# Performance work log

Hardware: AMD Instinct MI355X
Metric: run time of the kernel (lower is better)

Reference implementation:

```python
import jax, jax.numpy as jnp
import numpy as np

V, E, H, L, C = 50257, 256, 256, 2, 64
B, T = 4, 48
MASK_ID = 103
EPS = 1e-5
SAMPLE_KEY = jax.random.key(1234)


def lstm_cell(x, h, c, Wih, Whh, bih, bhh):
    # PyTorch gate order: i, f, g, o
    z = x @ Wih.T + h @ Whh.T + (bih + bhh)  # [B,4H]
    i, f, g, o = jnp.split(z, 4, axis=-1)
    c = jax.nn.sigmoid(f) * c + jax.nn.sigmoid(i) * jnp.tanh(g)
    h = jax.nn.sigmoid(o) * jnp.tanh(c)
    return h, c


def setup_inputs() -> dict:
    key = jax.random.key(0)
    ks = jax.random.split(key, 16)
    g = lambda k, s: (jax.random.normal(k, s, dtype=jnp.float32) * 0.05)
    emb = g(ks[0], (V, E)).at[0].set(0.0)  # padding_idx=0 row zeroed
    params = dict(
        emb=emb,
        W_e2e=g(ks[1], (H, E)), b_e2e=jnp.zeros((H,), jnp.float32),
        W_e2d=g(ks[2], (H, E)), b_e2d=jnp.zeros((H,), jnp.float32),
        enc_Wih=g(ks[3], (L, 4 * H, H)), enc_Whh=g(ks[4], (L, 4 * H, H)),
        enc_bih=jnp.zeros((L, 4 * H), jnp.float32), enc_bhh=jnp.zeros((L, 4 * H), jnp.float32),
        dec_Wih=g(ks[5], (L, 4 * H, H)), dec_Whh=g(ks[6], (L, 4 * H, H)),
        dec_bih=jnp.zeros((L, 4 * H), jnp.float32), dec_bhh=jnp.zeros((L, 4 * H), jnp.float32),
        W_cls=g(ks[7], (C, 1)), b_cls=jnp.zeros((C,), jnp.float32),
        W_fc1=g(ks[8], (H + C, H + C)), b_fc1=jnp.zeros((H + C,), jnp.float32),
        ln_g=jnp.ones((H + C,), jnp.float32), ln_b=jnp.zeros((H + C,), jnp.float32),
        W_fc2=g(ks[9], (V, H + C)), b_fc2=jnp.zeros((V,), jnp.float32),
    )
    input_ids = jax.random.randint(ks[10], (B, T), 0, V, dtype=jnp.int32)
    mask_pos = jax.random.bernoulli(ks[11], 0.3, (B, T))  # ensure masked slots exist
    input_ids = jnp.where(mask_pos, jnp.int32(MASK_ID), input_ids)
    attention_mask = jnp.ones((B, T), jnp.int32)
    classification_labels = jax.random.bernoulli(ks[12], 0.5, (B,)).astype(jnp.float32)
    return dict(input_ids=input_ids, attention_mask=attention_mask,
                classification_labels=classification_labels, **params)


def _forward(input_ids, classification_labels, emb, W_e2e, b_e2e, W_e2d, b_e2d,
             enc_Wih, enc_Whh, enc_bih, enc_bhh, dec_Wih, dec_Whh, dec_bih, dec_bhh,
             W_cls, b_cls, W_fc1, b_fc1, ln_g, ln_b, W_fc2, b_fc2):
    f32 = jnp.float32
    # ---- encoder: embed -> linear+relu (dropout=eval identity) -> 2-layer LSTM ----
    xe = jax.nn.relu(emb[input_ids] @ W_e2e.T + b_e2e)  # [B,T,H]
    xs = jnp.swapaxes(xe, 0, 1)  # [T,B,H]
    h0 = jnp.zeros((L, B, H), f32)

    def enc_step(hc, xj):
        h, c = hc
        cur, hs, cs = xj, [], []
        for l in range(L):
            nh, nc = lstm_cell(cur, h[l], c[l], enc_Wih[l], enc_Whh[l], enc_bih[l], enc_bhh[l])
            hs.append(nh); cs.append(nc); cur = nh
        return (jnp.stack(hs), jnp.stack(cs)), None

    (h, c), _ = jax.lax.scan(enc_step, (h0, h0), xs)

    # classifier states are loop-invariant in the original (hoisted, same math)
    cls_states = classification_labels[:, None] @ W_cls.T + b_cls  # [B,C]

    tokens0 = jnp.zeros((B, T), input_ids.dtype).at[:, 0].set(input_ids[:, 0])

    def decode_step(carry, t):
        tokens, h, c = carry
        # re-embed the ENTIRE current prefix, as the original does each step
        x = jax.nn.relu(emb[tokens] @ W_e2d.T + b_e2d)  # [B,T,H]
        xs_t = jnp.swapaxes(x, 0, 1)  # [T,B,H]

        def mstep(hc, inp):
            hh, cc = hc
            xj, j = inp
            cur, hs, cs = xj, [], []
            for l in range(L):
                nh, nc = lstm_cell(cur, hh[l], cc[l], dec_Wih[l], dec_Whh[l], dec_bih[l], dec_bhh[l])
                hs.append(nh); cs.append(nc); cur = nh
            nh, nc = jnp.stack(hs), jnp.stack(cs)
            valid = j < t  # only positions 0..t-1 are real prefix tokens
            hh = jnp.where(valid, nh, hh)
            cc = jnp.where(valid, nc, cc)
            return (hh, cc), hh[-1]

        (h, c), ys = jax.lax.scan(mstep, (h, c), (xs_t, jnp.arange(T)))
        dec_out = jax.lax.dynamic_index_in_dim(ys, t - 1, axis=0, keepdims=False)  # [B,H]

        z = jnp.concatenate([dec_out, cls_states], axis=-1)  # [B,H+C]
        z1 = jax.nn.relu(z @ W_fc1.T + b_fc1)
        mu = z1.mean(-1, keepdims=True)
        var = ((z1 - mu) ** 2).mean(-1, keepdims=True)
        z1 = (z1 - mu) * jax.lax.rsqrt(var + EPS) * ln_g + ln_b
        logits = z1 @ W_fc2.T + b_fc2  # [B,V]
        logp = jax.nn.log_softmax(logits, axis=-1)

        gumb = jax.random.gumbel(jax.random.fold_in(SAMPLE_KEY, t), logp.shape)
        sampled = jnp.argmax(logp + gumb, axis=-1)  # [B] categorical sample
        slp = jnp.take_along_axis(logp, sampled[:, None], axis=-1)[:, 0]  # [B]

        cur_tok = jnp.take(input_ids, t, axis=1)  # [B]
        next_tok = jnp.where(cur_tok == MASK_ID, sampled.astype(tokens.dtype), cur_tok)
        tokens = jax.lax.dynamic_update_slice(tokens, next_tok[:, None], (0, t))
        return (tokens, h, c), slp

    (tokens, h, c), slps = jax.lax.scan(decode_step, (tokens0, h, c), jnp.arange(1, T))
    scores = jnp.concatenate([jnp.zeros((B, 1), f32), slps.T], axis=1)  # [B,T]
    return scores, tokens


def reference(input_ids, attention_mask, classification_labels, emb, W_e2e, b_e2e,
              W_e2d, b_e2d, enc_Wih, enc_Whh, enc_bih, enc_bhh, dec_Wih, dec_Whh,
              dec_bih, dec_bhh, W_cls, b_cls, W_fc1, b_fc1, ln_g, ln_b, W_fc2, b_fc2):
    # attention_mask is accepted but unused, matching the original forward
    return _forward(input_ids, classification_labels, emb, W_e2e, b_e2e, W_e2d, b_e2d,
                    enc_Wih, enc_Whh, enc_bih, enc_bhh, dec_Wih, dec_Whh, dec_bih, dec_bhh,
                    W_cls, b_cls, W_fc1, b_fc1, ln_g, ln_b, W_fc2, b_fc2)
```

## Files before the change

kernel.cpp:

```cpp
#include <hip/hip_runtime.h>
#include <stdint.h>
#include <stddef.h>
#include <math.h>


#define PARTITIONABLE_PRNG 1

namespace s2sr {

constexpr int kV = 50257, kE = 256, kH = 256, kCc = 64, kB = 4, kT = 48;
constexpr int kZ = kH + kCc;
constexpr int kG = 4 * kH;
constexpr int kMask = 103;
constexpr float kEps = 1e-5f;
constexpr float kTiny = 1.17549435e-38f;

constexpr int NWG = 256, TPB = 256;
constexpr int NCL = 32;
constexpr int LEAD = 32;
constexpr int GANG0 = 33;
constexpr int NGANG = NWG - GANG0;
constexpr int RPW = (kV + NGANG - 1) / NGANG;
constexpr int NPX = 16;

constexpr int SH_H0 = 0;
constexpr int SH_H1 = 1024;
constexpr int SH_P0 = 2048;
constexpr int SH_P1 = 3072;
constexpr int SH_TOT = 4608;
constexpr int LD_ZIN = 0;
constexpr int LD_Z1  = 1280;
constexpr int LD_CLS = 2560;
constexpr int LD_LSE = 2816;
constexpr int LD_WPS = 2820;

struct alignas(128) Tag { unsigned v; unsigned _p[31]; };
struct alignas(128) GOut {
  unsigned long long key[kB];
  float ps[kB];
  unsigned tag;
  unsigned _p[19];
};

struct SyncBlk {
  Tag ictr, igen;
  Tag ptok4[NPX][4];
  Tag ztag4[4];
  Tag etok4[4];
  Tag hztag[NCL];
  GOut gout[NGANG];
};

struct WS {
  SyncBlk s;
  unsigned long long hc0[2][kB * kH];
  unsigned long long hc1[2][kB * kH];
  float hzbuf[2][kB][kH];
  float z1n[2][kB][kZ];
  float xcur[kB][kH];
  float xd0[kB][kH];
  float px0[kT][kB][kG];
  float pxe[kT][kB][kG];
};

__device__ __forceinline__ float aldf(const float* p) {
  return __hip_atomic_load(p, __ATOMIC_RELAXED, __HIP_MEMORY_SCOPE_AGENT);
}
__device__ __forceinline__ void astf(float* p, float v) {
  __hip_atomic_store(p, v, __ATOMIC_RELAXED, __HIP_MEMORY_SCOPE_AGENT);
}
__device__ __forceinline__ unsigned ldu(const unsigned* p) {
  return __hip_atomic_load(p, __ATOMIC_RELAXED, __HIP_MEMORY_SCOPE_AGENT);
}
__device__ __forceinline__ unsigned long long ld64(const unsigned long long* p) {
  return __hip_atomic_load(p, __ATOMIC_RELAXED, __HIP_MEMORY_SCOPE_AGENT);
}
__device__ __forceinline__ void st64(unsigned long long* p, unsigned long long v) {
  __hip_atomic_store(p, v, __ATOMIC_RELAXED, __HIP_MEMORY_SCOPE_AGENT);
}
__device__ __forceinline__ void relTag(Tag* tg, unsigned v) {
  __hip_atomic_store(&tg->v, v, __ATOMIC_RELEASE, __HIP_MEMORY_SCOPE_AGENT);
}
__device__ __forceinline__ void gbar(SyncBlk* sb, unsigned tgt) {
  __syncthreads();
  if (threadIdx.x == 0) {
    const unsigned old = __hip_atomic_fetch_add(&sb->ictr.v, 1u, __ATOMIC_RELEASE,
                                                __HIP_MEMORY_SCOPE_AGENT);
    if (old == tgt - 1u) relTag(&sb->igen, tgt);
    while (ldu(&sb->igen.v) < tgt) __builtin_amdgcn_s_sleep(2);
    __atomic_signal_fence(__ATOMIC_ACQUIRE);
  }
  __syncthreads();
}

__device__ __forceinline__ unsigned rotl32(unsigned v, int n) {
  return (v << n) | (v >> (32 - n));
}
__device__ __forceinline__ void tf2x32(unsigned k0, unsigned k1, unsigned x0, unsigned x1,
                                       unsigned& o0, unsigned& o1) {
  const unsigned k2 = k0 ^ k1 ^ 0x1BD11BDAu;
  unsigned v0 = x0 + k0, v1 = x1 + k1;
  v0 += v1; v1 = rotl32(v1, 13); v1 ^= v0;
  v0 += v1; v1 = rotl32(v1, 15); v1 ^= v0;
  v0 += v1; v1 = rotl32(v1, 26); v1 ^= v0;
  v0 += v1; v1 = rotl32(v1, 6);  v1 ^= v0;
  v0 += k1; v1 += k2 + 1u;
  v0 += v1; v1 = rotl32(v1, 17); v1 ^= v0;
  v0 += v1; v1 = rotl32(v1, 29); v1 ^= v0;
  v0 += v1; v1 = rotl32(v1, 16); v1 ^= v0;
  v0 += v1; v1 = rotl32(v1, 24); v1 ^= v0;
  v0 += k2; v1 += k0 + 2u;
  v0 += v1; v1 = rotl32(v1, 13); v1 ^= v0;
  v0 += v1; v1 = rotl32(v1, 15); v1 ^= v0;
  v0 += v1; v1 = rotl32(v1, 26); v1 ^= v0;
  v0 += v1; v1 = rotl32(v1, 6);  v1 ^= v0;
  v0 += k0; v1 += k1 + 3u;
  v0 += v1; v1 = rotl32(v1, 17); v1 ^= v0;
  v0 += v1; v1 = rotl32(v1, 29); v1 ^= v0;
  v0 += v1; v1 = rotl32(v1, 16); v1 ^= v0;
  v0 += v1; v1 = rotl32(v1, 24); v1 ^= v0;
  v0 += k1; v1 += k2 + 4u;
  v0 += v1; v1 = rotl32(v1, 13); v1 ^= v0;
  v0 += v1; v1 = rotl32(v1, 15); v1 ^= v0;
  v0 += v1; v1 = rotl32(v1, 26); v1 ^= v0;
  v0 += v1; v1 = rotl32(v1, 6);  v1 ^= v0;
  o0 = v0 + k2; o1 = v1 + k0 + 5u;
}
__device__ __forceinline__ unsigned rbits(unsigned k0, unsigned k1, unsigned i) {
#if PARTITIONABLE_PRNG
  unsigned a, b; tf2x32(k0, k1, 0u, i, a, b);
  return a ^ b;
#else
  constexpr unsigned HALF = (unsigned)((kB * kV + 1) / 2);
  unsigned a, b;
  if (i < HALF) { tf2x32(k0, k1, i, i + HALF, a, b); return a; }
  tf2x32(k0, k1, i - HALF, i, a, b); return b;
#endif
}
__device__ __forceinline__ float gumbel_from_bits(unsigned bits) {
  float f = __uint_as_float((bits >> 9) | 0x3f800000u) - 1.0f;
  f = fmaxf(f, kTiny);
  return -logf(-logf(f));
}
__device__ __forceinline__ unsigned ordkey(float f) {
  const unsigned u = __float_as_uint(f);
  return (u & 0x80000000u) ? ~u : (u | 0x80000000u);
}
__device__ __forceinline__ unsigned long long shflx64(unsigned long long v, int m) {
  unsigned lo = (unsigned)v, hi = (unsigned)(v >> 32);
  lo = (unsigned)__shfl_xor((int)lo, m, 64);
  hi = (unsigned)__shfl_xor((int)hi, m, 64);
  return ((unsigned long long)hi << 32) | (unsigned long long)lo;
}
__device__ __forceinline__ float sigm(float x) { return 1.0f / (1.0f + expf(-x)); }

template <bool STREAM>
__device__ __forceinline__ void lstm_tick(
    WS* ws, float* shf, int cw, int cc, bool do0, bool do1,
    const float* px, const float* pW0, const float* pW1,
    const float4* w0r, const float4* w1r,
    const float* bs0, const float* bs1,
    float& c0, float& c1, float& h0last, float& h1last,
    int w, int r, bool fin, int fu, int fb, int hzt) {
  const int tid = (int)threadIdx.x;
  float pxg0 = 0.f, pxg1 = 0.f, pxg2 = 0.f, pxg3 = 0.f;
  if (do0 && fin) {
    const float* pb = px + fb * kG + cw * 8 + fu;
    pxg0 = aldf(pb);
    pxg1 = aldf(pb + 256);
    pxg2 = aldf(pb + 512);
    pxg3 = aldf(pb + 768);
  }
  {
    const unsigned long long* base = &ws->hc0[(cc + 1) & 1][0];
    const unsigned expseq = (unsigned)cc;
    unsigned long long v[4];
#pragma unroll
    for (int k = 0; k < 4; ++k) v[k] = ld64(base + tid + k * 256);
    unsigned pend = 0;
#pragma unroll
    for (int k = 0; k < 4; ++k) if ((unsigned)v[k] != expseq) pend |= 1u << k;
    while (pend) {
#pragma unroll
      for (int k = 0; k < 4; ++k)
        if (pend & (1u << k)) v[k] = ld64(base + tid + k * 256);
#pragma unroll
      for (int k = 0; k < 4; ++k)
        if ((unsigned)v[k] == expseq) pend &= ~(1u << k);
    }
#pragma unroll
    for (int k = 0; k < 4; ++k)
      shf[SH_H0 + tid + k * 256] = __uint_as_float((unsigned)(v[k] >> 32));
  }
  __syncthreads();
  if (do0) {
    float4 wv0[8];
#pragma unroll
    for (int i = 0; i < 8; ++i)
      wv0[i] = STREAM ? *reinterpret_cast<const float4*>(pW0 + i * 4) : w0r[i];
    const float* A = &shf[SH_H0 + w * 32];
    float a0 = 0.f, a1 = 0.f, a2 = 0.f, a3 = 0.f;
#pragma unroll
    for (int i = 0; i < 8; ++i) {
      const float4 wv = wv0[i];
      const float4 x0 = *reinterpret_cast<const float4*>(A + 0 * 256 + i * 4);
      const float4 x1 = *reinterpret_cast<const float4*>(A + 1 * 256 + i * 4);
      const float4 x2 = *reinterpret_cast<const float4*>(A + 2 * 256 + i * 4);
      const float4 x3 = *reinterpret_cast<const float4*>(A + 3 * 256 + i * 4);
      a0 = fmaf(wv.x, x0.x, a0); a0 = fmaf(wv.y, x0.y, a0); a0 = fmaf(wv.z, x0.z, a0); a0 = fmaf(wv.w, x0.w, a0);
      a1 = fmaf(wv.x, x1.x, a1); a1 = fmaf(wv.y, x1.y, a1); a1 = fmaf(wv.z, x1.z, a1); a1 = fmaf(wv.w, x1.w, a1);
      a2 = fmaf(wv.x, x2.x, a2); a2 = fmaf(wv.y, x2.y, a2); a2 = fmaf(wv.z, x2.z, a2); a2 = fmaf(wv.w, x2.w, a2);
      a3 = fmaf(wv.x, x3.x, a3); a3 = fmaf(wv.y, x3.y, a3); a3 = fmaf(wv.z, x3.z, a3); a3 = fmaf(wv.w, x3.w, a3);
    }
    *reinterpret_cast<float4*>(&shf[SH_P0 + w * 128 + r * 4]) = float4{a0, a1, a2, a3};
  }
  __syncthreads();
  if (fin) {
    float hn = h0last;
    if (do0) {
      float z[4];
#pragma unroll
      for (int g = 0; g < 4; ++g) {
        const int base2 = SH_P0 + (fu * 4 + g) * 4 + fb;
        z[g] = shf[base2 + 0 * 128] + shf[base2 + 1 * 128] + shf[base2 + 2 * 128] +
               shf[base2 + 3 * 128] + shf[base2 + 4 * 128] + shf[base2 + 5 * 128] +
               shf[base2 + 6 * 128] + shf[base2 + 7 * 128] + bs0[g];
      }
      z[0] += pxg0; z[1] += pxg1; z[2] += pxg2; z[3] += pxg3;
      const float cn = sigm(z[1]) * c0 + sigm(z[0]) * tanhf(z[2]);
      hn = sigm(z[3]) * tanhf(cn);
      c0 = cn;
    }
    h0last = hn;
    st64(&ws->hc0[cc & 1][fb * 256 + cw * 8 + fu],
         ((unsigned long long)__float_as_uint(hn) << 32) |
         (unsigned long long)(unsigned)(cc + 1));
  }
  {
    const unsigned long long* base = &ws->hc1[(cc + 1) & 1][0];
    const unsigned expseq = (unsigned)cc;
    unsigned long long v[4];
#pragma unroll
    for (int k = 0; k < 4; ++k) v[k] = ld64(base + tid + k * 256);
    unsigned pend = 0;
#pragma unroll
    for (int k = 0; k < 4; ++k) if ((unsigned)v[k] != expseq) pend |= 1u << k;
    while (pend) {
#pragma unroll
      for (int k = 0; k < 4; ++k)
        if (pend & (1u << k)) v[k] = ld64(base + tid + k * 256);
#pragma unroll
      for (int k = 0; k < 4; ++k)
        if ((unsigned)v[k] == expseq) pend &= ~(1u << k);
    }
#pragma unroll
    for (int k = 0; k < 4; ++k)
      shf[SH_H1 + tid + k * 256] = __uint_as_float((unsigned)(v[k] >> 32));
  }
  __syncthreads();
  if (do1) {
    float4 wv1[16];
#pragma unroll
    for (int i = 0; i < 16; ++i)
      wv1[i] = STREAM ? *reinterpret_cast<const float4*>(pW1 + i * 4) : w1r[i];
    const float* Bp = (w < 4) ? &shf[SH_H0 + w * 64] : &shf[SH_H1 + (w - 4) * 64];
    float a0 = 0.f, a1 = 0.f, a2 = 0.f, a3 = 0.f;
#pragma unroll
    for (int i = 0; i < 16; ++i) {
      const float4 wv = wv1[i];
      const float4 x0 = *reinterpret_cast<const float4*>(Bp + 0 * 256 + i * 4);
      const float4 x1 = *reinterpret_cast<const float4*>(Bp + 1 * 256 + i * 4);
      const float4 x2 = *reinterpret_cast<const float4*>(Bp + 2 * 256 + i * 4);
      const float4 x3 = *reinterpret_cast<const float4*>(Bp + 3 * 256 + i * 4);
      a0 = fmaf(wv.x, x0.x, a0); a0 = fmaf(wv.y, x0.y, a0); a0 = fmaf(wv.z, x0.z, a0); a0 = fmaf(wv.w, x0.w, a0);
      a1 = fmaf(wv.x, x1.x, a1); a1 = fmaf(wv.y, x1.y, a1); a1 = fmaf(wv.z, x1.z, a1); a1 = fmaf(wv.w, x1.w, a1);
      a2 = fmaf(wv.x, x2.x, a2); a2 = fmaf(wv.y, x2.y, a2); a2 = fmaf(wv.z, x2.z, a2); a2 = fmaf(wv.w, x2.w, a2);
      a3 = fmaf(wv.x, x3.x, a3); a3 = fmaf(wv.y, x3.y, a3); a3 = fmaf(wv.z, x3.z, a3); a3 = fmaf(wv.w, x3.w, a3);
    }
    *reinterpret_cast<float4*>(&shf[SH_P1 + w * 128 + r * 4]) = float4{a0, a1, a2, a3};
  }
  __syncthreads();
  if (fin) {
    float hn = h1last;
    if (do1) {
      float z[4];
#pragma unroll
      for (int g = 0; g < 4; ++g) {
        const int base2 = SH_P1 + (fu * 4 + g) * 4 + fb;
        z[g] = shf[base2 + 0 * 128] + shf[base2 + 1 * 128] + shf[base2 + 2 * 128] +
               shf[base2 + 3 * 128] + shf[base2 + 4 * 128] + shf[base2 + 5 * 128] +
               shf[base2 + 6 * 128] + shf[base2 + 7 * 128] + bs1[g];
      }
      const float cn = sigm(z[1]) * c1 + sigm(z[0]) * tanhf(z[2]);
      hn = sigm(z[3]) * tanhf(cn);
      c1 = cn;
    }
    h1last = hn;
    st64(&ws->hc1[cc & 1][fb * 256 + cw * 8 + fu],
         ((unsigned long long)__float_as_uint(hn) << 32) |
         (unsigned long long)(unsigned)(cc + 1));
    if (hzt >= 0) astf(&ws->hzbuf[hzt & 1][fb][cw * 8 + fu], hn);
  }
}

__global__ void __launch_bounds__(TPB, 1) s2s_kernel(
    const int* __restrict__ input_ids, const float* __restrict__ labels,
    const float* __restrict__ emb,
    const float* __restrict__ W_e2e, const float* __restrict__ b_e2e,
    const float* __restrict__ W_e2d, const float* __restrict__ b_e2d,
    const float* __restrict__ encWih, const float* __restrict__ encWhh,
    const float* __restrict__ encbih, const float* __restrict__ encbhh,
    const float* __restrict__ decWih, const float* __restrict__ decWhh,
    const float* __restrict__ decbih, const float* __restrict__ decbhh,
    const float* __restrict__ W_cls, const float* __restrict__ b_cls,
    const float* __restrict__ Wfc1, const float* __restrict__ bfc1,
    const float* __restrict__ lng, const float* __restrict__ lnb,
    const float* __restrict__ W_fc2, const float* __restrict__ b_fc2,
    float* __restrict__ out, WS* __restrict__ ws) {
  const int wg = (int)blockIdx.x;
  const int tid = (int)threadIdx.x;
  SyncBlk* sb = &ws->s;
  __shared__ __align__(16) float shf[SH_TOT];
  __shared__ unsigned long long shk[16];
  __shared__ int shi[8];

  if (wg < kB * kT) {
    const int b = wg / kT, j = wg % kT;
    const int id = input_ids[b * kT + j];
    for (int i = tid; i < kE; i += 256) shf[i] = emb[(size_t)id * kE + i];
    __syncthreads();
    const float* wr = W_e2e + (size_t)tid * kE;
    float acc = b_e2e[tid];
    for (int k = 0; k < kE; k += 4) {
      const float4 wv = *reinterpret_cast<const float4*>(wr + k);
      const float4 xv = *reinterpret_cast<const float4*>(&shf[k]);
      acc = fmaf(xv.x, wv.x, acc); acc = fmaf(xv.y, wv.y, acc);
      acc = fmaf(xv.z, wv.z, acc); acc = fmaf(xv.w, wv.w, acc);
    }
    __syncthreads();
    shf[256 + tid] = fmaxf(acc, 0.f);
  } else if (wg == 192) {
    if (tid < kB) {
      const int t0 = input_ids[tid * kT];
      out[tid * kT] = 0.f;
      out[kB * kT + tid * kT] = (float)t0;
    }
  } else if (wg == 193) {
    const float* wr = W_e2d + (size_t)tid * kE;
    const float* e0 = emb + (size_t)input_ids[0 * kT] * kE;
    const float* e1 = emb + (size_t)input_ids[1 * kT] * kE;
    const float* e2 = emb + (size_t)input_ids[2 * kT] * kE;
    const float* e3 = emb + (size_t)input_ids[3 * kT] * kE;
    const float bb = b_e2d[tid];
    float a0 = bb, a1 = bb, a2 = bb, a3 = bb;
    for (int k = 0; k < kE; k += 4) {
      const float4 wv = *reinterpret_cast<const float4*>(wr + k);
      const float4 v0 = *reinterpret_cast<const float4*>(e0 + k);
      const float4 v1 = *reinterpret_cast<const float4*>(e1 + k);
      const float4 v2 = *reinterpret_cast<const float4*>(e2 + k);
      const float4 v3 = *reinterpret_cast<const float4*>(e3 + k);
      a0 = fmaf(v0.x, wv.x, a0); a0 = fmaf(v0.y, wv.y, a0); a0 = fmaf(v0.z, wv.z, a0); a0 = fmaf(v0.w, wv.w, a0);
      a1 = fmaf(v1.x, wv.x, a1); a1 = fmaf(v1.y, wv.y, a1); a1 = fmaf(v1.z, wv.z, a1); a1 = fmaf(v1.w, wv.w, a1);
      a2 = fmaf(v2.x, wv.x, a2); a2 = fmaf(v2.y, wv.y, a2); a2 = fmaf(v2.z, wv.z, a2); a2 = fmaf(v2.w, wv.w, a2);
      a3 = fmaf(v3.x, wv.x, a3); a3 = fmaf(v3.y, wv.y, a3); a3 = fmaf(v3.z, wv.z, a3); a3 = fmaf(v3.w, wv.w, a3);
    }
    astf(&ws->xd0[0][tid], fmaxf(a0, 0.f));
    astf(&ws->xd0[1][tid], fmaxf(a1, 0.f));
    astf(&ws->xd0[2][tid], fmaxf(a2, 0.f));
    astf(&ws->xd0[3][tid], fmaxf(a3, 0.f));
  }
  gbar(sb, (unsigned)NWG);

  if (wg < kB * kT) {
    const int b = wg / kT, j = wg % kT;
#pragma unroll
    for (int rr = 0; rr < 4; ++rr) {
      const int g = rr * 256 + tid;
      const float* wr = encWih + (size_t)g * kH;
      float acc = 0.f;
      for (int k = 0; k < kH; k += 4) {
        const float4 wv = *reinterpret_cast<const float4*>(wr + k);
        const float4 xv = *reinterpret_cast<const float4*>(&shf[256 + k]);
        acc = fmaf(xv.x, wv.x, acc); acc = fmaf(xv.y, wv.y, acc);
        acc = fmaf(xv.z, wv.z, acc); acc = fmaf(xv.w, wv.w, acc);
      }
      astf(&ws->pxe[j][0][0] + (size_t)b * kG + g, acc);
    }
  } else if (wg >= 192 && wg < 208) {
    const int w2 = wg - 192, b = w2 >> 2, q = w2 & 3;
    const int g = q * 256 + tid;
    for (int i = tid; i < kH; i += 256) shf[i] = aldf(&ws->xd0[b][i]);
    __syncthreads();
    const float* wr = decWih + (size_t)g * kH;
    float acc = 0.f;
    for (int k = 0; k < kH; k += 4) {
      const float4 wv = *reinterpret_cast<const float4*>(wr + k);
      const float4 xv = *reinterpret_cast<const float4*>(&shf[k]);
      acc = fmaf(xv.x, wv.x, acc); acc = fmaf(xv.y, wv.y, acc);
      acc = fmaf(xv.z, wv.z, acc); acc = fmaf(xv.w, wv.w, acc);
    }
    astf(&ws->px0[0][0][0] + (size_t)b * kG + g, acc);
  }
  gbar(sb, (unsigned)(2 * NWG));

  if (wg < NCL) {
    const int cw = wg;
    const int r = tid & 31, w = tid >> 5;
    const int grow = (r & 3) * 256 + cw * 8 + (r >> 2);
    const bool fin = tid < 32;
    const int fu = tid >> 2, fb = tid & 3;
    float c0 = 0.f, c1 = 0.f, h0last = 0.f, h1last = 0.f;
    float bs0[4] = {0.f, 0.f, 0.f, 0.f}, bs1[4] = {0.f, 0.f, 0.f, 0.f};
    if (fin) {
#pragma unroll
      for (int g = 0; g < 4; ++g) {
        bs0[g] = encbih[g * 256 + cw * 8 + fu] + encbhh[g * 256 + cw * 8 + fu];
        bs1[g] = encbih[kG + g * 256 + cw * 8 + fu] + encbhh[kG + g * 256 + cw * 8 + fu];
      }
    }
    const float* pW0e = encWhh + (size_t)grow * kH + w * 32;
    const float* pW1e = (w < 4)
        ? encWih + (size_t)kG * kH + (size_t)grow * kH + w * 64
        : encWhh + (size_t)kG * kH + (size_t)grow * kH + (w - 4) * 64;
    int cc = 0;
    for (int j = 0; j < kT; ++j, ++cc)
      lstm_tick<true>(ws, shf, cw, cc, true, j > 0, &ws->pxe[j][0][0],
                      pW0e, pW1e, nullptr, nullptr, bs0, bs1,
                      c0, c1, h0last, h1last, w, r, fin, fu, fb, -1);
    lstm_tick<true>(ws, shf, cw, cc, false, true, nullptr,
                    pW0e, pW1e, nullptr, nullptr, bs0, bs1,
                    c0, c1, h0last, h1last, w, r, fin, fu, fb, -1);
    ++cc;
    float4 w0d[8], w1d[16];
    {
      const float* p0 = decWhh + (size_t)grow * kH + w * 32;
#pragma unroll
      for (int i = 0; i < 8; ++i) w0d[i] = *reinterpret_cast<const float4*>(p0 + i * 4);
      const float* p1 = (w < 4)
          ? decWih + (size_t)kG * kH + (size_t)grow * kH + w * 64
          : decWhh + (size_t)kG * kH + (size_t)grow * kH + (w - 4) * 64;
#pragma unroll
      for (int i = 0; i < 16; ++i) w1d[i] = *reinterpret_cast<const float4*>(p1 + i * 4);
      if (fin) {
#pragma unroll
        for (int g = 0; g < 4; ++g) {
          bs0[g] = decbih[g * 256 + cw * 8 + fu] + decbhh[g * 256 + cw * 8 + fu];
          bs1[g] = decbih[kG + g * 256 + cw * 8 + fu] + decbhh[kG + g * 256 + cw * 8 + fu];
        }
      }
    }
    for (int t = 1; t < kT; ++t) {
      for (int j = 0; j < t; ++j, ++cc) {
        const bool d1 = (j > 0) || (t >= 2);
        const int hzt = (j == 0 && t >= 2) ? (t - 1) : -1;
        if (j == t - 1 && t >= 2) {
          if (tid < 64) {
            Tag* p = &sb->ptok4[tid >> 2][tid & 3];
            while (ldu(&p->v) < (unsigned)(t - 1)) {}
            __atomic_signal_fence(__ATOMIC_ACQUIRE);
          }
          __syncthreads();
        }
        lstm_tick<false>(ws, shf, cw, cc, true, d1, &ws->px0[j][0][0],
                         nullptr, nullptr, w0d, w1d, bs0, bs1,
                         c0, c1, h0last, h1last, w, r, fin, fu, fb, hzt);
        if (hzt >= 0 && tid == 0) relTag(&sb->hztag[cw], (unsigned)hzt);
      }
    }
    lstm_tick<false>(ws, shf, cw, cc, false, true, nullptr,
                     nullptr, nullptr, w0d, w1d, bs0, bs1,
                     c0, c1, h0last, h1last, w, r, fin, fu, fb, kT - 1);
    if (tid == 0) relTag(&sb->hztag[cw], (unsigned)(kT - 1));
  } else if (wg == LEAD) {
    if (tid < kB * kCc) {
      const int b = tid >> 6, c = tid & 63;
      shf[LD_CLS + tid] = fmaf(labels[b], W_cls[c], b_cls[c]);
    }
    __syncthreads();
    for (int t = 1; t < kT; ++t) {
      if (tid < NCL) {
        while (ldu(&sb->hztag[tid].v) < (unsigned)t) __builtin_amdgcn_s_sleep(1);
        __atomic_signal_fence(__ATOMIC_ACQUIRE);
      }
      __syncthreads();
      for (int i = tid; i < kB * kZ; i += 256) {
        const int b = i / kZ, k = i - b * kZ;
        shf[LD_ZIN + i] = (k < kH) ? aldf(&ws->hzbuf[t & 1][b][k])
                                   : shf[LD_CLS + b * kCc + (k - kH)];
      }
      __syncthreads();
#pragma unroll
      for (int rep = 0; rep < 5; ++rep) {
        const int task = tid + rep * 256;
        const int b = task / kZ, o = task - b * kZ;
        const float* wr = Wfc1 + (size_t)o * kZ;
        const float* zz = &shf[LD_ZIN + b * kZ];
        float acc = bfc1[o];
        for (int k = 0; k < kZ; k += 4) {
          const float4 wv = *reinterpret_cast<const float4*>(wr + k);
          const float4 zv = *reinterpret_cast<const float4*>(zz + k);
          acc = fmaf(zv.x, wv.x, acc); acc = fmaf(zv.y, wv.y, acc);
          acc = fmaf(zv.z, wv.z, acc); acc = fmaf(zv.w, wv.w, acc);
        }
        shf[LD_Z1 + task] = fmaxf(acc, 0.f);
      }
      __syncthreads();
      {
        const int b = tid >> 6, ln = tid & 63;
        float s1 = 0.f, s2 = 0.f;
        for (int i = ln; i < kZ; i += 64) {
          const float v2 = shf[LD_Z1 + b * kZ + i]; s1 += v2; s2 += v2 * v2;
        }
#pragma unroll
        for (int o = 32; o > 0; o >>= 1) { s1 += __shfl_xor(s1, o, 64); s2 += __shfl_xor(s2, o, 64); }
        const float mu = s1 * (1.0f / kZ);
        const float var = s2 * (1.0f / kZ) - mu * mu;
        const float rs = 1.0f / sqrtf(var + kEps);
        for (int i = ln; i < kZ; i += 64) {
          const float v2 = fmaf((shf[LD_Z1 + b * kZ + i] - mu) * rs, lng[i], lnb[i]);
          shf[LD_Z1 + b * kZ + i] = v2;
          astf(&ws->z1n[t & 1][b][i], v2);
        }
        if (ln == 0) relTag(&sb->ztag4[b], (unsigned)t);
      }
      if (tid < NGANG) {
        while (ldu(&sb->gout[tid].tag) < (unsigned)t) __builtin_amdgcn_s_sleep(2);
        __atomic_signal_fence(__ATOMIC_ACQUIRE);
      }
      __syncthreads();
      {
        unsigned long long kk[kB];
        float pp[kB];
        if (tid < NGANG) {
          const GOut* g = &sb->gout[tid];
#pragma unroll
          for (int b = 0; b < kB; ++b) { kk[b] = ld64(&g->key[b]); pp[b] = aldf(&g->ps[b]); }
        } else {
#pragma unroll
          for (int b = 0; b < kB; ++b) { kk[b] = 0ull; pp[b] = 0.f; }
        }
#pragma unroll
        for (int b = 0; b < kB; ++b) {
#pragma unroll
          for (int m = 1; m < 64; m <<= 1) {
            const unsigned long long ko = shflx64(kk[b], m);
            pp[b] += __shfl_xor(pp[b], m, 64);
            if (ko > kk[b]) kk[b] = ko;
          }
        }
        if ((tid & 63) == 0) {
          const int wv = tid >> 6;
#pragma unroll
          for (int b = 0; b < kB; ++b) { shk[wv * kB + b] = kk[b]; shf[LD_WPS + wv * kB + b] = pp[b]; }
        }
      }
      __syncthreads();
      if (tid < kB) {
        const int b = tid;
        unsigned long long key = shk[b];
        float s = shf[LD_WPS + b];
        for (int wv = 1; wv < 4; ++wv) {
          const unsigned long long ko = shk[wv * kB + b];
          if (ko > key) key = ko;
          s += shf[LD_WPS + wv * kB + b];
        }
        const int samp = (int)(0xFFFFFFFFu - (unsigned)(key & 0xFFFFFFFFull));
        const float lse = logf(s);
        const int cur = input_ids[b * kT + t];
        const int nxt = (cur == kMask) ? samp : cur;
        out[kB * kT + b * kT + t] = (float)nxt;
        shi[b] = nxt; shi[4 + b] = samp;
        shf[LD_LSE + b] = lse;
      }
      __syncthreads();
      if (t < kT - 1) {
        const float* wr = W_e2d + (size_t)tid * kE;
        const float* e0 = emb + (size_t)shi[0] * kE;
        const float* e1 = emb + (size_t)shi[1] * kE;
        const float* e2 = emb + (size_t)shi[2] * kE;
        const float* e3 = emb + (size_t)shi[3] * kE;
        const float bb = b_e2d[tid];
        float a0 = bb, a1 = bb, a2 = bb, a3 = bb;
        for (int k = 0; k < kE; k += 4) {
          const float4 wv = *reinterpret_cast<const float4*>(wr + k);
          const float4 v0 = *reinterpret_cast<const float4*>(e0 + k);
          const float4 v1 = *reinterpret_cast<const float4*>(e1 + k);
          const float4 v2 = *reinterpret_cast<const float4*>(e2 + k);
          const float4 v3 = *reinterpret_cast<const float4*>(e3 + k);
          a0 = fmaf(v0.x, wv.x, a0); a0 = fmaf(v0.y, wv.y, a0); a0 = fmaf(v0.z, wv.z, a0); a0 = fmaf(v0.w, wv.w, a0);
          a1 = fmaf(v1.x, wv.x, a1); a1 = fmaf(v1.y, wv.y, a1); a1 = fmaf(v1.z, wv.z, a1); a1 = fmaf(v1.w, wv.w, a1);
          a2 = fmaf(v2.x, wv.x, a2); a2 = fmaf(v2.y, wv.y, a2); a2 = fmaf(v2.z, wv.z, a2); a2 = fmaf(v2.w, wv.w, a2);
          a3 = fmaf(v3.x, wv.x, a3); a3 = fmaf(v3.y, wv.y, a3); a3 = fmaf(v3.z, wv.z, a3); a3 = fmaf(v3.w, wv.w, a3);
        }
        astf(&ws->xcur[0][tid], fmaxf(a0, 0.f));
        astf(&ws->xcur[1][tid], fmaxf(a1, 0.f));
        astf(&ws->xcur[2][tid], fmaxf(a2, 0.f));
        astf(&ws->xcur[3][tid], fmaxf(a3, 0.f));
        if ((tid & 63) == 0) relTag(&sb->etok4[tid >> 6], (unsigned)t);
      }
      {
        const int b = tid >> 6, lane = tid & 63;
        const int sp = shi[4 + b];
        const float* wr = W_fc2 + (size_t)sp * kZ;
        float acc = 0.f;
#pragma unroll
        for (int i = 0; i < 5; ++i)
          acc = fmaf(shf[LD_Z1 + b * kZ + lane + i * 64], wr[lane + i * 64], acc);
#pragma unroll
        for (int o = 32; o > 0; o >>= 1) acc += __shfl_xor(acc, o, 64);
        if (lane == 0) out[b * kT + t] = acc + b_fc2[sp] - shf[LD_LSE + b];
      }
      __syncthreads();
    }
  } else {
    const int gi = wg - GANG0;
    const int start = gi * RPW;
    const int cnt = (RPW < kV - start) ? RPW : (kV - start);
    const bool act = tid < cnt;
    const int row = start + tid;
    for (int t = 1; t < kT; ++t) {
      if (tid < 4) {
        while (ldu(&sb->ztag4[tid].v) < (unsigned)t) __builtin_amdgcn_s_sleep(16);
        __atomic_signal_fence(__ATOMIC_ACQUIRE);
      }
      __syncthreads();
      for (int i = tid; i < kB * kZ; i += 256) shf[i] = aldf(&ws->z1n[t & 1][0][0] + i);
      __syncthreads();
      unsigned fk0, fk1;
      tf2x32(0u, 1234u, 0u, (unsigned)t, fk0, fk1);
      float lv[kB] = {0.f, 0.f, 0.f, 0.f};
      if (act) {
        const float* wr = W_fc2 + (size_t)row * kZ;
        const float bb = b_fc2[row];
// ... 119 lines not shown
```

Before: 6.969 ms.

## Split LSTM layers onto separate workgroup groups and pipeline them across ticks

```diff
diff --git a/kernel.cpp b/kernel.cpp
--- a/kernel.cpp
+++ b/kernel.cpp
@@ -16,7 +16,8 @@
 constexpr float kTiny = 1.17549435e-38f;
 
 constexpr int NWG = 256, TPB = 256;
-constexpr int NCL = 32;
+constexpr int NCL0 = 16;
+constexpr int NCL1 = 16;
 constexpr int LEAD = 32;
 constexpr int GANG0 = 33;
 constexpr int NGANG = NWG - GANG0;
@@ -25,8 +26,7 @@
 
 constexpr int SH_H0 = 0;
 constexpr int SH_H1 = 1024;
-constexpr int SH_P0 = 2048;
-constexpr int SH_P1 = 3072;
+constexpr int SH_P  = 2048;
 constexpr int SH_TOT = 4608;
 constexpr int LD_ZIN = 0;
 constexpr int LD_Z1  = 1280;
@@ -47,14 +47,14 @@
   Tag ptok4[NPX][4];
   Tag ztag4[4];
   Tag etok4[4];
-  Tag hztag[NCL];
+  Tag hztag[NCL1];
   GOut gout[NGANG];
 };
 
 struct WS {
   SyncBlk s;
-  unsigned long long hc0[2][kB * kH];
-  unsigned long long hc1[2][kB * kH];
+  unsigned long long hc0[4][kB * kH];
+  unsigned long long hc1[4][kB * kH];
   float hzbuf[2][kB][kH];
   float z1n[2][kB][kZ];
   float xcur[kB][kH];
@@ -154,65 +154,77 @@
 }
 __device__ __forceinline__ float sigm(float x) { return 1.0f / (1.0f + expf(-x)); }
 
+__device__ __forceinline__ void spin_stage(const unsigned long long* base,
+                                           unsigned expseq, float* shf, int dst) {
+  const int tid = (int)threadIdx.x;
+  unsigned long long v[4];
+#pragma unroll
+  for (int k = 0; k < 4; ++k) v[k] = ld64(base + tid + k * 256);
+  unsigned pend = 0;
+#pragma unroll
+  for (int k = 0; k < 4; ++k) if ((unsigned)v[k] != expseq) pend |= 1u << k;
+  while (pend) {
+#pragma unroll
+    for (int k = 0; k < 4; ++k)
+      if (pend & (1u << k)) v[k] = ld64(base + tid + k * 256);
+#pragma unroll
+    for (int k = 0; k < 4; ++k)
+      if ((unsigned)v[k] == expseq) pend &= ~(1u << k);
+  }
+#pragma unroll
+  for (int k = 0; k < 4; ++k)
+    shf[dst + tid + k * 256] = __uint_as_float((unsigned)(v[k] >> 32));
+}
+
 template <bool STREAM>
-__device__ __forceinline__ void lstm_tick(
-    WS* ws, float* shf, int cw, int cc, bool do0, bool do1,
-    const float* px, const float* pW0, const float* pW1,
-    const float4* w0r, const float4* w1r,
-    const float* bs0, const float* bs1,
-    float& c0, float& c1, float& h0last, float& h1last,
-    int w, int r, bool fin, int fu, int fb, int hzt) {
+__device__ __forceinline__ void l0_tick(
+    WS* ws, float* shf, int cw, int cc, bool do0, const float* px,
+    const float* pW0a, const float* pW0b, const float4* w0a, const float4* w0b,
+    const float* bs0, float& c0, float& h0last,
+    int r, int v, bool fin, int fu, int fb) {
   const int tid = (int)threadIdx.x;
   float pxg0 = 0.f, pxg1 = 0.f, pxg2 = 0.f, pxg3 = 0.f;
   if (do0 && fin) {
-    const float* pb = px + fb * kG + cw * 8 + fu;
+    const float* pb = px + fb * kG + cw * 16 + fu;
     pxg0 = aldf(pb);
     pxg1 = aldf(pb + 256);
     pxg2 = aldf(pb + 512);
     pxg3 = aldf(pb + 768);
   }
-  {
-    const unsigned long long* base = &ws->hc0[(cc + 1) & 1][0];
-    const unsigned expseq = (unsigned)cc;
-    unsigned long long v[4];
-#pragma unroll
-    for (int k = 0; k < 4; ++k) v[k] = ld64(base + tid + k * 256);
-    unsigned pend = 0;
-#pragma unroll
-    for (int k = 0; k < 4; ++k) if ((unsigned)v[k] != expseq) pend |= 1u << k;
-    while (pend) {
-#pragma unroll
-      for (int k = 0; k < 4; ++k)
-        if (pend & (1u << k)) v[k] = ld64(base + tid + k * 256);
-#pragma unroll
-      for (int k = 0; k < 4; ++k)
-        if ((unsigned)v[k] == expseq) pend &= ~(1u << k);
-    }
-#pragma unroll
-    for (int k = 0; k < 4; ++k)
-      shf[SH_H0 + tid + k * 256] = __uint_as_float((unsigned)(v[k] >> 32));
-  }
+  if (cc >= 3 && tid < NCL1) {
+    const unsigned long long* cr = &ws->hc1[(cc - 3) & 3][tid * 16];
+    const unsigned need = (unsigned)(cc - 2);
+    while ((unsigned)ld64(cr) < need) {}
+  }
+  spin_stage(&ws->hc0[(cc - 1) & 3][0], (unsigned)cc, shf, SH_H0);
   __syncthreads();
   if (do0) {
-    float4 wv0[8];
-#pragma unroll
-    for (int i = 0; i < 8; ++i)
-      wv0[i] = STREAM ? *reinterpret_cast<const float4*>(pW0 + i * 4) : w0r[i];
-    const float* A = &shf[SH_H0 + w * 32];
-    float a0 = 0.f, a1 = 0.f, a2 = 0.f, a3 = 0.f;
+    float4 wa[8], wb[8];
 #pragma unroll
     for (int i = 0; i < 8; ++i) {
-      const float4 wv = wv0[i];
-      const float4 x0 = *reinterpret_cast<const float4*>(A + 0 * 256 + i * 4);
-      const float4 x1 = *reinterpret_cast<const float4*>(A + 1 * 256 + i * 4);
-      const float4 x2 = *reinterpret_cast<const float4*>(A + 2 * 256 + i * 4);
-      const float4 x3 = *reinterpret_cast<const float4*>(A + 3 * 256 + i * 4);
-      a0 = fmaf(wv.x, x0.x, a0); a0 = fmaf(wv.y, x0.y, a0); a0 = fmaf(wv.z, x0.z, a0); a0 = fmaf(wv.w, x0.w, a0);
-      a1 = fmaf(wv.x, x1.x, a1); a1 = fmaf(wv.y, x1.y, a1); a1 = fmaf(wv.z, x1.z, a1); a1 = fmaf(wv.w, x1.w, a1);
-      a2 = fmaf(wv.x, x2.x, a2); a2 = fmaf(wv.y, x2.y, a2); a2 = fmaf(wv.z, x2.z, a2); a2 = fmaf(wv.w, x2.w, a2);
-      a3 = fmaf(wv.x, x3.x, a3); a3 = fmaf(wv.y, x3.y, a3); a3 = fmaf(wv.z, x3.z, a3); a3 = fmaf(wv.w, x3.w, a3);
-    }
-    *reinterpret_cast<float4*>(&shf[SH_P0 + w * 128 + r * 4]) = float4{a0, a1, a2, a3};
+      wa[i] = STREAM ? *reinterpret_cast<const float4*>(pW0a + i * 4) : w0a[i];
+      wb[i] = STREAM ? *reinterpret_cast<const float4*>(pW0b + i * 4) : w0b[i];
+    }
+#pragma unroll
+    for (int ww = 0; ww < 2; ++ww) {
+      const int W = ww ? (v + 4) : v;
+      const float4* wv_ = ww ? wb : wa;
+      const float* A = &shf[SH_H0 + W * 32];
+      float a0 = 0.f, a1 = 0.f, a2 = 0.f, a3 = 0.f;
+#pragma unroll
+      for (int i = 0; i < 8; ++i) {
+        const float4 wv = wv_[i];
+        const float4 x0 = *reinterpret_cast<const float4*>(A + 0 * 256 + i * 4);
+        const float4 x1 = *reinterpret_cast<const float4*>(A + 1 * 256 + i * 4);
+        const float4 x2 = *reinterpret_cast<const float4*>(A + 2 * 256 + i * 4);
+        const float4 x3 = *reinterpret_cast<const float4*>(A + 3 * 256 + i * 4);
+        a0 = fmaf(wv.x, x0.x, a0); a0 = fmaf(wv.y, x0.y, a0); a0 = fmaf(wv.z, x0.z, a0); a0 = fmaf(wv.w, x0.w, a0);
+        a1 = fmaf(wv.x, x1.x, a1); a1 = fmaf(wv.y, x1.y, a1); a1 = fmaf(wv.z, x1.z, a1); a1 = fmaf(wv.w, x1.w, a1);
+        a2 = fmaf(wv.x, x2.x, a2); a2 = fmaf(wv.y, x2.y, a2); a2 = fmaf(wv.z, x2.z, a2); a2 = fmaf(wv.w, x2.w, a2);
+        a3 = fmaf(wv.x, x3.x, a3); a3 = fmaf(wv.y, x3.y, a3); a3 = fmaf(wv.z, x3.z, a3); a3 = fmaf(wv.w, x3.w, a3);
+      }
+      *reinterpret_cast<float4*>(&shf[SH_P + W * 256 + r * 4]) = float4{a0, a1, a2, a3};
+    }
   }
   __syncthreads();
   if (fin) {
@@ -221,10 +233,11 @@
       float z[4];
 #pragma unroll
       for (int g = 0; g < 4; ++g) {
-        const int base2 = SH_P0 + (fu * 4 + g) * 4 + fb;
-        z[g] = shf[base2 + 0 * 128] + shf[base2 + 1 * 128] + shf[base2 + 2 * 128] +
-               shf[base2 + 3 * 128] + shf[base2 + 4 * 128] + shf[base2 + 5 * 128] +
-               shf[base2 + 6 * 128] + shf[base2 + 7 * 128] + bs0[g];
+        const int rw = (g * 16 + fu) * 4 + fb;
+        float s = 0.f;
+#pragma unroll
+        for (int W = 0; W < 8; ++W) s += shf[SH_P + W * 256 + rw];
+        z[g] = s + bs0[g];
       }
       z[0] += pxg0; z[1] += pxg1; z[2] += pxg2; z[3] += pxg3;
       const float cn = sigm(z[1]) * c0 + sigm(z[0]) * tanhf(z[2]);
@@ -232,52 +245,48 @@
       c0 = cn;
     }
     h0last = hn;
-    st64(&ws->hc0[cc & 1][fb * 256 + cw * 8 + fu],
+    st64(&ws->hc0[cc & 3][fb * 256 + cw * 16 + fu],
          ((unsigned long long)__float_as_uint(hn) << 32) |
          (unsigned long long)(unsigned)(cc + 1));
   }
-  {
-    const unsigned long long* base = &ws->hc1[(cc + 1) & 1][0];
-    const unsigned expseq = (unsigned)cc;
-    unsigned long long v[4];
-#pragma unroll
-    for (int k = 0; k < 4; ++k) v[k] = ld64(base + tid + k * 256);
-    unsigned pend = 0;
-#pragma unroll
-    for (int k = 0; k < 4; ++k) if ((unsigned)v[k] != expseq) pend |= 1u << k;
-    while (pend) {
-#pragma unroll
-      for (int k = 0; k < 4; ++k)
-        if (pend & (1u << k)) v[k] = ld64(base + tid + k * 256);
-#pragma unroll
-      for (int k = 0; k < 4; ++k)
-        if ((unsigned)v[k] == expseq) pend &= ~(1u << k);
-    }
-#pragma unroll
-    for (int k = 0; k < 4; ++k)
-      shf[SH_H1 + tid + k * 256] = __uint_as_float((unsigned)(v[k] >> 32));
-  }
+}
+
+template <bool STREAM>
+__device__ __forceinline__ void l1_tick(
+    WS* ws, float* shf, int cw, int cc, bool do1,
+    const float* pW1a, const float* pW1b, const float4* w1a, const float4* w1b,
+    const float* bs1, float& c1, float& h1last,
+    int r, int v, bool fin, int fu, int fb, int hzt) {
+  spin_stage(&ws->hc0[(cc - 1) & 3][0], (unsigned)cc, shf, SH_H0);
+  spin_stage(&ws->hc1[(cc - 1) & 3][0], (unsigned)cc, shf, SH_H1);
   __syncthreads();
   if (do1) {
-    float4 wv1[16];
-#pragma unroll
-    for (int i = 0; i < 16; ++i)
-      wv1[i] = STREAM ? *reinterpret_cast<const float4*>(pW1 + i * 4) : w1r[i];
-    const float* Bp = (w < 4) ? &shf[SH_H0 + w * 64] : &shf[SH_H1 + (w - 4) * 64];
-    float a0 = 0.f, a1 = 0.f, a2 = 0.f, a3 = 0.f;
+    float4 wa[16], wb[16];
 #pragma unroll
     for (int i = 0; i < 16; ++i) {
-      const float4 wv = wv1[i];
-      const float4 x0 = *reinterpret_cast<const float4*>(Bp + 0 * 256 + i * 4);
-      const float4 x1 = *reinterpret_cast<const float4*>(Bp + 1 * 256 + i * 4);
-      const float4 x2 = *reinterpret_cast<const float4*>(Bp + 2 * 256 + i * 4);
-      const float4 x3 = *reinterpret_cast<const float4*>(Bp + 3 * 256 + i * 4);
-      a0 = fmaf(wv.x, x0.x, a0); a0 = fmaf(wv.y, x0.y, a0); a0 = fmaf(wv.z, x0.z, a0); a0 = fmaf(wv.w, x0.w, a0);
-      a1 = fmaf(wv.x, x1.x, a1); a1 = fmaf(wv.y, x1.y, a1); a1 = fmaf(wv.z, x1.z, a1); a1 = fmaf(wv.w, x1.w, a1);
-      a2 = fmaf(wv.x, x2.x, a2); a2 = fmaf(wv.y, x2.y, a2); a2 = fmaf(wv.z, x2.z, a2); a2 = fmaf(wv.w, x2.w, a2);
-      a3 = fmaf(wv.x, x3.x, a3); a3 = fmaf(wv.y, x3.y, a3); a3 = fmaf(wv.z, x3.z, a3); a3 = fmaf(wv.w, x3.w, a3);
-    }
-    *reinterpret_cast<float4*>(&shf[SH_P1 + w * 128 + r * 4]) = float4{a0, a1, a2, a3};
+      wa[i] = STREAM ? *reinterpret_cast<const float4*>(pW1a + i * 4) : w1a[i];
+      wb[i] = STREAM ? *reinterpret_cast<const float4*>(pW1b + i * 4) : w1b[i];
+    }
+#pragma unroll
+    for (int ww = 0; ww < 2; ++ww) {
+      const int W = ww ? (v + 4) : v;
+      const float4* wv_ = ww ? wb : wa;
+      const float* Bp = (W < 4) ? &shf[SH_H0 + W * 64] : &shf[SH_H1 + (W - 4) * 64];
+      float a0 = 0.f, a1 = 0.f, a2 = 0.f, a3 = 0.f;
+#pragma unroll
+      for (int i = 0; i < 16; ++i) {
+        const float4 wv = wv_[i];
+        const float4 x0 = *reinterpret_cast<const float4*>(Bp + 0 * 256 + i * 4);
+        const float4 x1 = *reinterpret_cast<const float4*>(Bp + 1 * 256 + i * 4);
+        const float4 x2 = *reinterpret_cast<const float4*>(Bp + 2 * 256 + i * 4);
+        const float4 x3 = *reinterpret_cast<const float4*>(Bp + 3 * 256 + i * 4);
+        a0 = fmaf(wv.x, x0.x, a0); a0 = fmaf(wv.y, x0.y, a0); a0 = fmaf(wv.z, x0.z, a0); a0 = fmaf(wv.w, x0.w, a0);
+        a1 = fmaf(wv.x, x1.x, a1); a1 = fmaf(wv.y, x1.y, a1); a1 = fmaf(wv.z, x1.z, a1); a1 = fmaf(wv.w, x1.w, a1);
+        a2 = fmaf(wv.x, x2.x, a2); a2 = fmaf(wv.y, x2.y, a2); a2 = fmaf(wv.z, x2.z, a2); a2 = fmaf(wv.w, x2.w, a2);
+        a3 = fmaf(wv.x, x3.x, a3); a3 = fmaf(wv.y, x3.y, a3); a3 = fmaf(wv.z, x3.z, a3); a3 = fmaf(wv.w, x3.w, a3);
+      }
+      *reinterpret_cast<float4*>(&shf[SH_P + W * 256 + r * 4]) = float4{a0, a1, a2, a3};
+    }
   }
   __syncthreads();
   if (fin) {
@@ -286,20 +295,21 @@
       float z[4];
 #pragma unroll
       for (int g = 0; g < 4; ++g) {
-        const int base2 = SH_P1 + (fu * 4 + g) * 4 + fb;
-        z[g] = shf[base2 + 0 * 128] + shf[base2 + 1 * 128] + shf[base2 + 2 * 128] +
-               shf[base2 + 3 * 128] + shf[base2 + 4 * 128] + shf[base2 + 5 * 128] +
-               shf[base2 + 6 * 128] + shf[base2 + 7 * 128] + bs1[g];
+        const int rw = (g * 16 + fu) * 4 + fb;
+        float s = 0.f;
+#pragma unroll
+        for (int W = 0; W < 8; ++W) s += shf[SH_P + W * 256 + rw];
+        z[g] = s + bs1[g];
       }
       const float cn = sigm(z[1]) * c1 + sigm(z[0]) * tanhf(z[2]);
       hn = sigm(z[3]) * tanhf(cn);
       c1 = cn;
     }
     h1last = hn;
-    st64(&ws->hc1[cc & 1][fb * 256 + cw * 8 + fu],
+    st64(&ws->hc1[cc & 3][fb * 256 + cw * 16 + fu],
          ((unsigned long long)__float_as_uint(hn) << 32) |
          (unsigned long long)(unsigned)(cc + 1));
-    if (hzt >= 0) astf(&ws->hzbuf[hzt & 1][fb][cw * 8 + fu], hn);
+    if (hzt >= 0) astf(&ws->hzbuf[hzt & 1][fb][cw * 16 + fu], hn);
   }
 }
 
@@ -403,56 +413,45 @@
   }
   gbar(sb, (unsigned)(2 * NWG));
 
-  if (wg < NCL) {
+  if (wg < NCL0) {
     const int cw = wg;
-    const int r = tid & 31, w = tid >> 5;
-    const int grow = (r & 3) * 256 + cw * 8 + (r >> 2);
-    const bool fin = tid < 32;
+    const int r = tid & 63, v = tid >> 6;
+    const int grow = (r >> 4) * 256 + cw * 16 + (r & 15);
+    const bool fin = tid < 64;
     const int fu = tid >> 2, fb = tid & 3;
-    float c0 = 0.f, c1 = 0.f, h0last = 0.f, h1last = 0.f;
-    float bs0[4] = {0.f, 0.f, 0.f, 0.f}, bs1[4] = {0.f, 0.f, 0.f, 0.f};
+    float c0 = 0.f, h0last = 0.f;
+    float bs0[4] = {0.f, 0.f, 0.f, 0.f};
     if (fin) {
 #pragma unroll
-      for (int g = 0; g < 4; ++g) {
-        bs0[g] = encbih[g * 256 + cw * 8 + fu] + encbhh[g * 256 + cw * 8 + fu];
-        bs1[g] = encbih[kG + g * 256 + cw * 8 + fu] + encbhh[kG + g * 256 + cw * 8 + fu];
-      }
-    }
-    const float* pW0e = encWhh + (size_t)grow * kH + w * 32;
-    const float* pW1e = (w < 4)
-        ? encWih + (size_t)kG * kH + (size_t)grow * kH + w * 64
-        : encWhh + (size_t)kG * kH + (size_t)grow * kH + (w - 4) * 64;
+      for (int g = 0; g < 4; ++g)
+        bs0[g] = encbih[g * 256 + cw * 16 + fu] + encbhh[g * 256 + cw * 16 + fu];
+    }
+    const float* pW0a = encWhh + (size_t)grow * kH + v * 32;
+    const float* pW0b = encWhh + (size_t)grow * kH + (v + 4) * 32;
     int cc = 0;
     for (int j = 0; j < kT; ++j, ++cc)
-      lstm_tick<true>(ws, shf, cw, cc, true, j > 0, &ws->pxe[j][0][0],
-                      pW0e, pW1e, nullptr, nullptr, bs0, bs1,
-                      c0, c1, h0last, h1last, w, r, fin, fu, fb, -1);
-    lstm_tick<true>(ws, shf, cw, cc, false, true, nullptr,
-                    pW0e, pW1e, nullptr, nullptr, bs0, bs1,
-                    c0, c1, h0last, h1last, w, r, fin, fu, fb, -1);
+      l0_tick<true>(ws, shf, cw, cc, true, &ws->pxe[j][0][0],
+                    pW0a, pW0b, nullptr, nullptr, bs0, c0, h0last, r, v, fin, fu, fb);
+    l0_tick<true>(ws, shf, cw, cc, false, nullptr,
+                  pW0a, pW0b, nullptr, nullptr, bs0, c0, h0last, r, v, fin, fu, fb);
     ++cc;
-    float4 w0d[8], w1d[16];
+    float4 w0a[8], w0b[8];
     {
-      const float* p0 = decWhh + (size_t)grow * kH + w * 32;
-#pragma unroll
-      for (int i = 0; i < 8; ++i) w0d[i] = *reinterpret_cast<const float4*>(p0 + i * 4);
-      const float* p1 = (w < 4)
-          ? decWih + (size_t)kG * kH + (size_t)grow * kH + w * 64
-          : decWhh + (size_t)kG * kH + (size_t)grow * kH + (w - 4) * 64;
-#pragma unroll
-      for (int i = 0; i < 16; ++i) w1d[i] = *reinterpret_cast<const float4*>(p1 + i * 4);
+      const float* pa = decWhh + (size_t)grow * kH + v * 32;
+      const float* pb = decWhh + (size_t)grow * kH + (v + 4) * 32;
+#pragma unroll
+      for (int i = 0; i < 8; ++i) {
+        w0a[i] = *reinterpret_cast<const float4*>(pa + i * 4);
+        w0b[i] = *reinterpret_cast<const float4*>(pb + i * 4);
+      }
       if (fin) {
 #pragma unroll
-        for (int g = 0; g < 4; ++g) {
-          bs0[g] = decbih[g * 256 + cw * 8 + fu] + decbhh[g * 256 + cw * 8 + fu];
-          bs1[g] = decbih[kG + g * 256 + cw * 8 + fu] + decbhh[kG + g * 256 + cw * 8 + fu];
-        }
+        for (int g = 0; g < 4; ++g)
+          bs0[g] = decbih[g * 256 + cw * 16 + fu] + decbhh[g * 256 + cw * 16 + fu];
       }
     }
     for (int t = 1; t < kT; ++t) {
       for (int j = 0; j < t; ++j, ++cc) {
-        const bool d1 = (j > 0) || (t >= 2);
-        const int hzt = (j == 0 && t >= 2) ? (t - 1) : -1;
         if (j == t - 1 && t >= 2) {
           if (tid < 64) {
             Tag* p = &sb->ptok4[tid >> 2][tid & 3];
@@ -461,15 +460,58 @@
           }
           __syncthreads();
         }
-        lstm_tick<false>(ws, shf, cw, cc, true, d1, &ws->px0[j][0][0],
-                         nullptr, nullptr, w0d, w1d, bs0, bs1,
-                         c0, c1, h0last, h1last, w, r, fin, fu, fb, hzt);
+        l0_tick<false>(ws, shf, cw, cc, true, &ws->px0[j][0][0],
+                       nullptr, nullptr, w0a, w0b, bs0, c0, h0last, r, v, fin, fu, fb);
+      }
+    }
+  } else if (wg < NCL0 + NCL1) {
+    const int cw = wg - NCL0;
+    const int r = tid & 63, v = tid >> 6;
+    const int grow = (r >> 4) * 256 + cw * 16 + (r & 15);
+    const bool fin = tid < 64;
+    const int fu = tid >> 2, fb = tid & 3;
+    float c1 = 0.f, h1last = 0.f;
+    float bs1[4] = {0.f, 0.f, 0.f, 0.f};
+    if (fin) {
+#pragma unroll
+      for (int g = 0; g < 4; ++g)
+        bs1[g] = encbih[kG + g * 256 + cw * 16 + fu] + encbhh[kG + g * 256 + cw * 16 + fu];
+    }
+    const float* pW1a = encWih + (size_t)kG * kH + (size_t)grow * kH + v * 64;
+    const float* pW1b = encWhh + (size_t)kG * kH + (size_t)grow * kH + v * 64;
+    int cc = 0;
+    for (int j = 0; j < kT; ++j, ++cc)
+      l1_tick<true>(ws, shf, cw, cc, j > 0, pW1a, pW1b, nullptr, nullptr,
+                    bs1, c1, h1last, r, v, fin, fu, fb, -1);
+    l1_tick<true>(ws, shf, cw, cc, true, pW1a, pW1b, nullptr, nullptr,
+                  bs1, c1, h1last, r, v, fin, fu, fb, -1);
+    ++cc;
+    float4 w1a[16], w1b[16];
+    {
+      const float* pa = decWih + (size_t)kG * kH + (size_t)grow * kH + v * 64;
+      const float* pb = decWhh + (size_t)kG * kH + (size_t)grow * kH + v * 64;
+#pragma unroll
+      for (int i = 0; i < 16; ++i) {
+        w1a[i] = *reinterpret_cast<const float4*>(pa + i * 4);
+        w1b[i] = *reinterpret_cast<const float4*>(pb + i * 4);
+      }
+      if (fin) {
+#pragma unroll
+        for (int g = 0; g < 4; ++g)
+          bs1[g] = decbih[kG + g * 256 + cw * 16 + fu] + decbhh[kG + g * 256 + cw * 16 + fu];
+      }
+    }
+    for (int t = 1; t < kT; ++t) {
+      for (int j = 0; j < t; ++j, ++cc) {
+        const bool d1 = (j > 0) || (t >= 2);
+        const int hzt = (j == 0 && t >= 2) ? (t - 1) : -1;
+        l1_tick<false>(ws, shf, cw, cc, d1, nullptr, nullptr, w1a, w1b,
+                       bs1, c1, h1last, r, v, fin, fu, fb, hzt);
         if (hzt >= 0 && tid == 0) relTag(&sb->hztag[cw], (unsigned)hzt);
       }
     }
-    lstm_tick<false>(ws, shf, cw, cc, false, true, nullptr,
-                     nullptr, nullptr, w0d, w1d, bs0, bs1,
-                     c0, c1, h0last, h1last, w, r, fin, fu, fb, kT - 1);
+    l1_tick<false>(ws, shf, cw, cc, true, nullptr, nullptr, w1a, w1b,
+                   bs1, c1, h1last, r, v, fin, fu, fb, kT - 1);
     if (tid == 0) relTag(&sb->hztag[cw], (unsigned)(kT - 1));
   } else if (wg == LEAD) {
     if (tid < kB * kCc) {
@@ -478,7 +520,7 @@
     }
     __syncthreads();
     for (int t = 1; t < kT; ++t) {
-      if (tid < NCL) {
+      if (tid < NCL1) {
         while (ldu(&sb->hztag[tid].v) < (unsigned)t) __builtin_amdgcn_s_sleep(1);
         __atomic_signal_fence(__ATOMIC_ACQUIRE);
       }
```

Result: slower. 8.149 ms (+16.9%).
